# Optimization experiments

Measured on AMD Instinct MI355X. Metric: run time of the kernel, lower is better.

The kernel has to match this reference:

```python
import jax, jax.numpy as jnp
import numpy as np

N_ATOMS = 512
N_MOL = 16
HIDDEN = 128
FILTERS = 128
NUM_RBF = 50
CUTOFF = 10.0
N_LAYERS = 3


def setup_inputs() -> dict:
    key = jax.random.key(0)
    ks = jax.random.split(key, 20)
    s = 0.05
    inp = {
        "atomic_numbers": jax.random.randint(ks[0], (N_ATOMS,), 0, 100),
        "positions": jax.random.uniform(ks[1], (N_ATOMS, 3), jnp.float32) * CUTOFF,
        "batch": jnp.sort(jax.random.randint(ks[2], (N_ATOMS,), 0, N_MOL)),
        # parameters (linear weights stored as [in, out])
        "emb": jax.random.normal(ks[3], (100, HIDDEN), jnp.float32) * s,
        "fw1": jax.random.normal(ks[4], (N_LAYERS, NUM_RBF, FILTERS), jnp.float32) * s,
        "fb1": jnp.zeros((N_LAYERS, FILTERS), jnp.float32),
        "fw2": jax.random.normal(ks[5], (N_LAYERS, FILTERS, FILTERS), jnp.float32) * s,
        "fb2": jnp.zeros((N_LAYERS, FILTERS), jnp.float32),
        "d1w": jax.random.normal(ks[6], (N_LAYERS, HIDDEN, FILTERS), jnp.float32) * s,
        "d1b": jnp.zeros((N_LAYERS, FILTERS), jnp.float32),
        "d2w": jax.random.normal(ks[7], (N_LAYERS, FILTERS, HIDDEN), jnp.float32) * s,
        "d2b": jnp.zeros((N_LAYERS, HIDDEN), jnp.float32),
        "ow1": jax.random.normal(ks[8], (HIDDEN, HIDDEN // 2), jnp.float32) * s,
        "ob1": jnp.zeros((HIDDEN // 2,), jnp.float32),
        "ow2": jax.random.normal(ks[9], (HIDDEN // 2, 1), jnp.float32) * s,
        "ob2": jnp.zeros((1,), jnp.float32),
    }
    return inp


def _schnet_fwd(atomic_numbers, positions, batch, emb, fw1, fb1, fw2, fb2,
                d1w, d1b, d2w, d2b, ow1, ob1, ow2, ob2):
    N = positions.shape[0]
    x = emb[atomic_numbers]                                  # [N, H]

    # all-pairs distances (safe sqrt for the zero diagonal)
    diff = positions[:, None, :] - positions[None, :, :]     # [N, N, 3]
    d2 = jnp.sum(diff * diff, axis=-1)                       # [N, N]
    d = jnp.sqrt(jnp.where(d2 > 0, d2, 1.0))
    d = jnp.where(d2 > 0, d, 0.0)

    eye = jnp.eye(N, dtype=bool)
    valid = (~eye) & (d < CUTOFF)                            # no self-edges, within cutoff

    # gaussian RBF embedding of distances
    centers = jnp.linspace(0.0, CUTOFF, NUM_RBF)             # [R]
    width = CUTOFF / NUM_RBF
    rbf = jnp.exp(-((d[..., None] - centers) ** 2) / (2.0 * width * width))  # [N, N, R]

    # cosine cutoff envelope; zero on invalid edges -> messages identical to edge-list version
    env = 0.5 * (jnp.cos(d * jnp.pi / CUTOFF) + 1.0) * valid.astype(d.dtype)  # [N, N]

    for l in range(N_LAYERS):
        filt = jax.nn.silu(rbf @ fw1[l] + fb1[l]) @ fw2[l] + fb2[l]   # [N, N, F]
        filt = filt * env[..., None]
        xj = x @ d1w[l] + d1b[l]                                      # [N, F] source features
        # message[i,j] = xj[i] * filt[i,j]; scatter-add to destination j
        agg = jnp.einsum('if,ijf->jf', xj, filt)                      # [N, F]
        x = x + agg @ d2w[l] + d2b[l]

    # mean-pool atoms per molecule
    mol_sum = jax.ops.segment_sum(x, batch, num_segments=N_MOL)       # [M, H]
    counts = jax.ops.segment_sum(jnp.ones((N,), x.dtype), batch, num_segments=N_MOL)
    mol = mol_sum / jnp.clip(counts, 1.0)[:, None]

    h = jax.nn.silu(mol @ ow1 + ob1)
    return h @ ow2 + ob2                                              # [M, 1]


def reference(atomic_numbers, positions, batch, emb, fw1, fb1, fw2, fb2,
              d1w, d1b, d2w, d2b, ow1, ob1, ow2, ob2):
    return _schnet_fwd(atomic_numbers, positions, batch, emb, fw1, fb1, fw2, fb2,
                       d1w, d1b, d2w, d2b, ow1, ob1, ow2, ob2)
```

## Files before the change

### kernel.cpp

```cpp
#include <hip/hip_runtime.h>
#include <math.h>

#define N_ATOMS 512
#define N_MOL   16
#define HIDDEN  128
#define FILTERS 128
#define NUM_RBF 50
#define CUTOFF  10.0f
#define N_LAYERS 3

#define KB2    2048
#define NB2    (KB2 + 1)
#define TBPL   65
#define TBLK   (N_LAYERS * TBPL)
#define EMBB   16
#define PI_F   3.14159265358979f
#define DINV   204.8f
#define DSTEP  (CUTOFF / (float)KB2)
#define TAB_U4 ((NB2 * 64) / 4)

__device__ __forceinline__ unsigned short f2bf(float v) {
    unsigned u = __float_as_uint(v);
    u += 0x7fffu + ((u >> 16) & 1u);
    return (unsigned short)(u >> 16);
}

__global__ void __launch_bounds__(256) k_front(
        const int* __restrict__ an, const float* __restrict__ emb,
        const float* __restrict__ d1w, const float* __restrict__ d1b,
        const float* __restrict__ fw1, const float* __restrict__ fb1,
        const float* __restrict__ fw2, const float* __restrict__ fb2,
        float* __restrict__ x, unsigned short* __restrict__ xj,
        unsigned short* __restrict__ tab, float* __restrict__ molsum,
        int* __restrict__ done) {
    __shared__ float s_rbf[32][NUM_RBF];
    __shared__ __align__(16) float s_H[32][132];
    __shared__ __align__(16) float s_row[32][HIDDEN];
    __shared__ int   s_an[32];
    int bid = blockIdx.x, t = threadIdx.x;

    if (bid == 0) {
        for (int idx = t; idx < N_MOL * HIDDEN; idx += 256) molsum[idx] = 0.f;
        if (t < 4) done[t] = 0;
    }

    int cq = t & 31, ag = t >> 5;

    if (bid < TBLK) {
        int l = bid / TBPL, bx = bid - l * TBPL;
        int bin0 = bx * 32;
        const float* w1g = fw1 + (size_t)l * NUM_RBF * FILTERS;
        const float* w2g = fw2 + (size_t)l * FILTERS * FILTERS;
        for (int idx = t; idx < 32 * NUM_RBF; idx += 256) {
            int lb = idx / NUM_RBF, r = idx - lb * NUM_RBF;
            float dd = (bin0 + lb) * DSTEP;
            float cr = r * (CUTOFF / (float)(NUM_RBF - 1));
            float xx = dd - cr;
            s_rbf[lb][r] = __expf(-xx * xx * 12.5f);
        }
        __syncthreads();
        {
            float h[4][4];
            float4 bv = *(const float4*)(fb1 + (size_t)l * FILTERS + 4 * cq);
            float bva[4] = { bv.x, bv.y, bv.z, bv.w };
            #pragma unroll
            for (int aa = 0; aa < 4; aa++)
                #pragma unroll
                for (int cc = 0; cc < 4; cc++) h[aa][cc] = bva[cc];
            #pragma unroll 2
            for (int r = 0; r < NUM_RBF; r++) {
                float4 w = *(const float4*)(w1g + (size_t)r * FILTERS + 4 * cq);
                float wa[4] = { w.x, w.y, w.z, w.w };
                #pragma unroll
                for (int aa = 0; aa < 4; aa++) {
                    float rb = s_rbf[ag * 4 + aa][r];
                    #pragma unroll
                    for (int cc = 0; cc < 4; cc++) h[aa][cc] = fmaf(rb, wa[cc], h[aa][cc]);
                }
            }
            __syncthreads();
            #pragma unroll
            for (int aa = 0; aa < 4; aa++) {
                float4 sv;
                sv.x = h[aa][0] / (1.f + __expf(-h[aa][0]));
                sv.y = h[aa][1] / (1.f + __expf(-h[aa][1]));
                sv.z = h[aa][2] / (1.f + __expf(-h[aa][2]));
                sv.w = h[aa][3] / (1.f + __expf(-h[aa][3]));
                *(float4*)(&s_H[ag * 4 + aa][4 * cq]) = sv;
            }
        }
        __syncthreads();
        float o[4][4];
        float4 b2v = *(const float4*)(fb2 + (size_t)l * FILTERS + 4 * cq);
        float b2a[4] = { b2v.x, b2v.y, b2v.z, b2v.w };
        #pragma unroll
        for (int aa = 0; aa < 4; aa++)
            #pragma unroll
            for (int cc = 0; cc < 4; cc++) o[aa][cc] = b2a[cc];
        #pragma unroll 4
        for (int hh = 0; hh < FILTERS; hh += 2) {
            float4 wA = *(const float4*)(w2g + (size_t)hh * FILTERS + 4 * cq);
            float4 wB = *(const float4*)(w2g + (size_t)(hh + 1) * FILTERS + 4 * cq);
            float wa[4] = { wA.x, wA.y, wA.z, wA.w };
            float wb[4] = { wB.x, wB.y, wB.z, wB.w };
            #pragma unroll
            for (int aa = 0; aa < 4; aa++) {
                float2 hp = *(const float2*)(&s_H[ag * 4 + aa][hh]);
                #pragma unroll
                for (int cc = 0; cc < 4; cc++) {
                    o[aa][cc] = fmaf(hp.x, wa[cc], o[aa][cc]);
                    o[aa][cc] = fmaf(hp.y, wb[cc], o[aa][cc]);
                }
            }
        }
        size_t base = (size_t)l * NB2 * FILTERS;
        #pragma unroll
        for (int aa = 0; aa < 4; aa++) {
            int bin = bin0 + ag * 4 + aa;
            if (bin <= KB2) {
                float dd = bin * DSTEP;
                float env = (bin >= KB2) ? 0.f : 0.5f * (__cosf(dd * (PI_F / CUTOFF)) + 1.f);
                #pragma unroll
                for (int cp = 0; cp < 2; cp++) {
                    unsigned int pk = (unsigned)f2bf(o[aa][2 * cp] * env) |
                                      ((unsigned)f2bf(o[aa][2 * cp + 1] * env) << 16);
                    *(unsigned int*)(tab + base + (size_t)bin * FILTERS + 4 * cq + 2 * cp) = pk;
                }
            }
        }
    } else {
        int eb = bid - TBLK;
        int i0 = eb * 32;
        if (t < 32) s_an[t] = an[i0 + t];
        __syncthreads();
        for (int idx = t; idx < 32 * HIDDEN; idx += 256) {
            int a = idx >> 7, c = idx & 127;
            float v = emb[(size_t)s_an[a] * HIDDEN + c];
            s_row[a][c] = v;
            x[(size_t)(i0 + a) * HIDDEN + c] = v;
        }
        __syncthreads();
        float o[4][4];
        float4 bv = *(const float4*)(d1b + 4 * cq);
        float bva[4] = { bv.x, bv.y, bv.z, bv.w };
        #pragma unroll
        for (int aa = 0; aa < 4; aa++)
            #pragma unroll
            for (int cc = 0; cc < 4; cc++) o[aa][cc] = bva[cc];
        #pragma unroll 4
        for (int h = 0; h < HIDDEN; h += 2) {
            float4 wA = *(const float4*)(d1w + (size_t)h * FILTERS + 4 * cq);
            float4 wB = *(const float4*)(d1w + (size_t)(h + 1) * FILTERS + 4 * cq);
            float wa[4] = { wA.x, wA.y, wA.z, wA.w };
            float wb[4] = { wB.x, wB.y, wB.z, wB.w };
            #pragma unroll
            for (int aa = 0; aa < 4; aa++) {
                float2 hp = *(const float2*)(&s_row[ag * 4 + aa][h]);
                #pragma unroll
                for (int cc = 0; cc < 4; cc++) {
                    o[aa][cc] = fmaf(hp.x, wa[cc], o[aa][cc]);
                    o[aa][cc] = fmaf(hp.y, wb[cc], o[aa][cc]);
                }
            }
        }
        #pragma unroll
        for (int aa = 0; aa < 4; aa++) {
            int i = i0 + ag * 4 + aa;
            #pragma unroll
            for (int cp = 0; cp < 2; cp++) {
                unsigned int pk = (unsigned)f2bf(o[aa][2 * cp]) |
                                  ((unsigned)f2bf(o[aa][2 * cp + 1]) << 16);
                *(unsigned int*)(xj + (size_t)i * FILTERS + 4 * cq + 2 * cp) = pk;
            }
        }
    }
}

template<int LAST>
__global__ void __launch_bounds__(512) k_layer(const float* __restrict__ pos,
        const unsigned int* __restrict__ tabl, const unsigned int* __restrict__ xj_in,
        float* __restrict__ x, const float* __restrict__ w2, const float* __restrict__ b2,
        const float* __restrict__ w1n, const float* __restrict__ b1n,
        unsigned int* __restrict__ xj_out,
        const int* __restrict__ batch, float* __restrict__ molsum, int* __restrict__ done,
        const float* __restrict__ ow1, const float* __restrict__ ob1,
        const float* __restrict__ ow2, const float* __restrict__ ob2,
        float* __restrict__ out) {
    int j = blockIdx.x, t = threadIdx.x;
    int wv = t >> 6, e = t & 63;
    __shared__ unsigned short s_bin[N_ATOMS];
    __shared__ float s_part[8][FILTERS];
    __shared__ float s_red[4][FILTERS];
    __shared__ float s_agg[FILTERS];
    __shared__ float s_xn[HIDDEN];
    __shared__ int   s_tick;
    __shared__ float s_mol[16][HIDDEN];
    __shared__ float s_h[16][64];
    __shared__ int   s_c16[16];
    {
        float px = pos[3*t], py = pos[3*t+1], pz = pos[3*t+2];
        float ax = pos[3*j], ay = pos[3*j+1], az = pos[3*j+2];
        float d = sqrtf((px-ax)*(px-ax) + (py-ay)*(py-ay) + (pz-az)*(pz-az));
        unsigned int b = (t == j || d >= CUTOFF) ? KB2 : (unsigned)(int)fmaf(d, DINV, 0.5f);
        if (b > KB2) b = KB2;
        s_bin[t] = (unsigned short)b;
    }
    int c = t & 127, seg = t >> 7;
    float xold = (seg == 0) ? x[(size_t)j * HIDDEN + c] : 0.f;
    {
        const uint4* t4 = (const uint4*)tabl;
        int slice = (j >> 3) & 31;
        int q0 = slice * 1025;
        int qe = q0 + 1025; if (qe > TAB_U4) qe = TAB_U4;
        unsigned int acc = 0;
        for (int q = q0 + t; q < qe; q += 512) {
            uint4 w = t4[q];
            acc ^= w.x ^ w.y ^ w.z ^ w.w;
        }
        asm volatile("" :: "v"(acc));
    }
    __syncthreads();
    float ae = 0.f, ao = 0.f;
    int i0 = wv * 64;
    for (int ii = 0; ii < 64; ii += 8) {
        #pragma unroll
        for (int r = 0; r < 8; r++) {
            int bb = s_bin[i0 + ii + r];
            unsigned int xu = xj_in[(size_t)(i0 + ii + r) * 64 + e];
            unsigned int f  = tabl[(size_t)bb * 64 + e];
            float xe = __uint_as_float(xu << 16), xo = __uint_as_float(xu & 0xffff0000u);
            float pe = __uint_as_float(f << 16),  po = __uint_as_float(f & 0xffff0000u);
            ae = fmaf(xe, pe, ae);
            ao = fmaf(xo, po, ao);
        }
    }
    s_part[wv][2*e] = ae;  s_part[wv][2*e+1] = ao;
    __syncthreads();
    if (t < FILTERS) {
        float s = 0.f;
        #pragma unroll
        for (int w8 = 0; w8 < 8; w8++) s += s_part[w8][t];
        s_agg[t] = s;
    }
    __syncthreads();
    float v = 0.f;
    #pragma unroll 8
    for (int ff = seg * 32; ff < seg * 32 + 32; ff++)
        v = fmaf(s_agg[ff], w2[(size_t)ff * HIDDEN + c], v);
    s_red[seg][c] = v;
    __syncthreads();
    float xnew = 0.f;
    if (seg == 0) {
        xnew = xold + b2[c] + s_red[0][c] + s_red[1][c] + s_red[2][c] + s_red[3][c];
        x[(size_t)j * HIDDEN + c] = xnew;
        s_xn[c] = xnew;
    }
    __syncthreads();
    if (!LAST) {
        float a2 = 0.f;
        #pragma unroll 8
        for (int hh = seg * 32; hh < seg * 32 + 32; hh++)
            a2 = fmaf(s_xn[hh], w1n[(size_t)hh * FILTERS + c], a2);
        s_red[seg][c] = a2;
        __syncthreads();
        if (t < 64) {
            float v0 = b1n[2*t]   + s_red[0][2*t]   + s_red[1][2*t]   + s_red[2][2*t]   + s_red[3][2*t];
            float v1 = b1n[2*t+1] + s_red[0][2*t+1] + s_red[1][2*t+1] + s_red[2][2*t+1] + s_red[3][2*t+1];
            xj_out[(size_t)j * 64 + t] = (unsigned)f2bf(v0) | ((unsigned)f2bf(v1) << 16);
        }
    } else {
        if (seg == 0) atomicAdd(&molsum[(size_t)batch[j] * HIDDEN + c], xnew);
        __syncthreads();
        if (t == 0) s_tick = atomicAdd(&done[0], 1);
        __syncthreads();
        if (s_tick == (int)gridDim.x - 1) {
            if (t < 16) s_c16[t] = 0;
            __syncthreads();
            atomicAdd(&s_c16[batch[t]], 1);
            __syncthreads();
            #pragma unroll
            for (int mo = 0; mo < 4; mo++) {
                int m = mo * 4 + seg;
                float sv = atomicAdd(&molsum[(size_t)m * HIDDEN + c], 0.f);
                int cnt = s_c16[m];
                s_mol[m][c] = sv / (float)(cnt > 0 ? cnt : 1);
            }
            __syncthreads();
            #pragma unroll
            for (int rr = 0; rr < 2; rr++) {
                int o = t + rr * 512;
                int m = o >> 6, k = o & 63;
                float a = ob1[k];
                #pragma unroll 8
                for (int h = 0; h < HIDDEN; h++) a = fmaf(s_mol[m][h], ow1[h * 64 + k], a);
                s_h[m][k] = a / (1.f + __expf(-a));
            }
            __syncthreads();
            if (t < N_MOL) {
                float a = ob2[0];
                #pragma unroll 8
                for (int h = 0; h < 64; h++) a = fmaf(s_h[t][h], ow2[h], a);
                out[t] = a;
            }
        }
    }
}

extern "C" void kernel_launch(void* const* d_in, const int* in_sizes, int n_in,
                              void* d_out, int out_size, void* d_ws, size_t ws_size,
                              hipStream_t stream) {
    const int*   an    = (const int*)  d_in[0];
    const float* pos   = (const float*)d_in[1];
    const int*   batch = (const int*)  d_in[2];
    const float* emb   = (const float*)d_in[3];
    const float* fw1   = (const float*)d_in[4];
    const float* fb1   = (const float*)d_in[5];
    const float* fw2   = (const float*)d_in[6];
    const float* fb2   = (const float*)d_in[7];
    const float* d1w   = (const float*)d_in[8];
    const float* d1b   = (const float*)d_in[9];
    const float* d2w   = (const float*)d_in[10];
    const float* d2b   = (const float*)d_in[11];
    const float* ow1   = (const float*)d_in[12];
    const float* ob1   = (const float*)d_in[13];
    const float* ow2   = (const float*)d_in[14];
    const float* ob2   = (const float*)d_in[15];
    float* out = (float*)d_out;

    float*          x    = (float*)d_ws;
    unsigned int*   xj0  = (unsigned int*)(x + N_ATOMS * HIDDEN);
    unsigned int*   xj1  = xj0 + (size_t)N_ATOMS * 64;
    unsigned int*   xj2  = xj1 + (size_t)N_ATOMS * 64;
    unsigned short* tab  = (unsigned short*)(xj2 + (size_t)N_ATOMS * 64);
    float*          mols = (float*)(tab + (size_t)N_LAYERS * NB2 * FILTERS);
    int*            done = (int*)(mols + N_MOL * HIDDEN);

    k_front<<<TBLK + EMBB, 256, 0, stream>>>(
        an, emb, d1w, d1b, fw1, fb1, fw2, fb2, x, (unsigned short*)xj0, tab, mols, done);

    const unsigned int* t0 = (const unsigned int*)(tab + (size_t)0 * NB2 * FILTERS);
    const unsigned int* t1 = (const unsigned int*)(tab + (size_t)1 * NB2 * FILTERS);
    const unsigned int* t2 = (const unsigned int*)(tab + (size_t)2 * NB2 * FILTERS);

    k_layer<0><<<N_ATOMS, 512, 0, stream>>>(pos, t0, xj0, x,
        d2w + (size_t)0*FILTERS*HIDDEN, d2b + (size_t)0*HIDDEN,
        d1w + (size_t)1*HIDDEN*FILTERS, d1b + (size_t)1*FILTERS, xj1,
        batch, mols, done, ow1, ob1, ow2, ob2, out);
    k_layer<0><<<N_ATOMS, 512, 0, stream>>>(pos, t1, xj1, x,
        d2w + (size_t)1*FILTERS*HIDDEN, d2b + (size_t)1*HIDDEN,
        d1w + (size_t)2*HIDDEN*FILTERS, d1b + (size_t)2*FILTERS, xj2,
        batch, mols, done, ow1, ob1, ow2, ob2, out);
    k_layer<1><<<N_ATOMS, 512, 0, stream>>>(pos, t2, xj2, x,
        d2w + (size_t)2*FILTERS*HIDDEN, d2b + (size_t)2*HIDDEN,
        d1w, d1b, xj0,
        batch, mols, done, ow1, ob1, ow2, ob2, out);
}
```

Measured before the change: 59.54 us.

## Halve filter lookup table resolution and widen per-lane gather loads

Cuts the precomputed per-distance filter table from 2048 to 1024 bins, so fewer table blocks are launched and each layer's table footprint (and prefetch slice) is halved. The aggregation loop now has each lane load 8-byte uint2 chunks covering four filter channels, with two half-waves processing alternating source atoms and combining through a cross-lane shuffle. Coarser binning adds interpolation error to the distance-dependent filter, in exchange for less table construction work and more cache-friendly gathers.

```diff
diff --git a/kernel.cpp b/kernel.cpp
--- a/kernel.cpp
+++ b/kernel.cpp
@@ -9,21 +9,23 @@
 #define CUTOFF  10.0f
 #define N_LAYERS 3
 
-#define KB2    2048
-#define NB2    (KB2 + 1)
-#define TBPL   65
+#define KB1    1024
+#define NB1    (KB1 + 1)
+#define TBPL   33
 #define TBLK   (N_LAYERS * TBPL)
 #define EMBB   16
 #define PI_F   3.14159265358979f
-#define DINV   204.8f
-#define DSTEP  (CUTOFF / (float)KB2)
-#define TAB_U4 ((NB2 * 64) / 4)
+#define DINV   102.4f
+#define DSTEP  (CUTOFF / (float)KB1)
+#define TAB_U4 ((NB1 * FILTERS * 2) / 16)
 
 __device__ __forceinline__ unsigned short f2bf(float v) {
     unsigned u = __float_as_uint(v);
     u += 0x7fffu + ((u >> 16) & 1u);
     return (unsigned short)(u >> 16);
 }
+__device__ __forceinline__ float bflo(unsigned int u) { return __uint_as_float(u << 16); }
+__device__ __forceinline__ float bfhi(unsigned int u) { return __uint_as_float(u & 0xffff0000u); }
 
 __global__ void __launch_bounds__(256) k_front(
         const int* __restrict__ an, const float* __restrict__ emb,
@@ -113,13 +115,13 @@
                 }
             }
         }
-        size_t base = (size_t)l * NB2 * FILTERS;
+        size_t base = (size_t)l * NB1 * FILTERS;
         #pragma unroll
         for (int aa = 0; aa < 4; aa++) {
             int bin = bin0 + ag * 4 + aa;
-            if (bin <= KB2) {
+            if (bin <= KB1) {
                 float dd = bin * DSTEP;
-                float env = (bin >= KB2) ? 0.f : 0.5f * (__cosf(dd * (PI_F / CUTOFF)) + 1.f);
+                float env = (bin >= KB1) ? 0.f : 0.5f * (__cosf(dd * (PI_F / CUTOFF)) + 1.f);
                 #pragma unroll
                 for (int cp = 0; cp < 2; cp++) {
                     unsigned int pk = (unsigned)f2bf(o[aa][2 * cp] * env) |
@@ -201,17 +203,17 @@
         float px = pos[3*t], py = pos[3*t+1], pz = pos[3*t+2];
         float ax = pos[3*j], ay = pos[3*j+1], az = pos[3*j+2];
         float d = sqrtf((px-ax)*(px-ax) + (py-ay)*(py-ay) + (pz-az)*(pz-az));
-        unsigned int b = (t == j || d >= CUTOFF) ? KB2 : (unsigned)(int)fmaf(d, DINV, 0.5f);
-        if (b > KB2) b = KB2;
+        unsigned int b = (t == j || d >= CUTOFF) ? KB1 : (unsigned)(int)fmaf(d, DINV, 0.5f);
+        if (b > KB1) b = KB1;
         s_bin[t] = (unsigned short)b;
     }
     int c = t & 127, seg = t >> 7;
     float xold = (seg == 0) ? x[(size_t)j * HIDDEN + c] : 0.f;
     {
         const uint4* t4 = (const uint4*)tabl;
-        int slice = (j >> 3) & 31;
-        int q0 = slice * 1025;
-        int qe = q0 + 1025; if (qe > TAB_U4) qe = TAB_U4;
+        int slice = j & 31;
+        int q0 = slice * 513;
+        int qe = q0 + 513; if (qe > TAB_U4) qe = TAB_U4;
         unsigned int acc = 0;
         for (int q = q0 + t; q < qe; q += 512) {
             uint4 w = t4[q];
@@ -220,21 +222,36 @@
         asm volatile("" :: "v"(acc));
     }
     __syncthreads();
-    float ae = 0.f, ao = 0.f;
-    int i0 = wv * 64;
-    for (int ii = 0; ii < 64; ii += 8) {
-        #pragma unroll
-        for (int r = 0; r < 8; r++) {
-            int bb = s_bin[i0 + ii + r];
-            unsigned int xu = xj_in[(size_t)(i0 + ii + r) * 64 + e];
-            unsigned int f  = tabl[(size_t)bb * 64 + e];
-            float xe = __uint_as_float(xu << 16), xo = __uint_as_float(xu & 0xffff0000u);
-            float pe = __uint_as_float(f << 16),  po = __uint_as_float(f & 0xffff0000u);
-            ae = fmaf(xe, pe, ae);
-            ao = fmaf(xo, po, ao);
-        }
-    }
-    s_part[wv][2*e] = ae;  s_part[wv][2*e+1] = ao;
+    {
+        int h = e >> 5, cq4 = e & 31;
+        const uint2* tb2 = (const uint2*)tabl;
+        const uint2* xj2 = (const uint2*)xj_in;
+        float a0 = 0.f, a1 = 0.f, a2 = 0.f, a3 = 0.f;
+        int i0 = wv * 64;
+        for (int ii = 0; ii < 64; ii += 8) {
+            #pragma unroll
+            for (int r = 0; r < 8; r += 2) {
+                int i = i0 + ii + r + h;
+                int bb = s_bin[i];
+                uint2 f  = tb2[(size_t)bb * 32 + cq4];
+                uint2 xu = xj2[(size_t)i  * 32 + cq4];
+                a0 = fmaf(bflo(xu.x), bflo(f.x), a0);
+                a1 = fmaf(bfhi(xu.x), bfhi(f.x), a1);
+                a2 = fmaf(bflo(xu.y), bflo(f.y), a2);
+                a3 = fmaf(bfhi(xu.y), bfhi(f.y), a3);
+            }
+        }
+        a0 += __shfl_down(a0, 32, 64);
+        a1 += __shfl_down(a1, 32, 64);
+        a2 += __shfl_down(a2, 32, 64);
+        a3 += __shfl_down(a3, 32, 64);
+        if (h == 0) {
+            s_part[wv][4*cq4+0] = a0;
+            s_part[wv][4*cq4+1] = a1;
+            s_part[wv][4*cq4+2] = a2;
+            s_part[wv][4*cq4+3] = a3;
+        }
+    }
     __syncthreads();
     if (t < FILTERS) {
         float s = 0.f;
@@ -332,15 +349,15 @@
     unsigned int*   xj1  = xj0 + (size_t)N_ATOMS * 64;
     unsigned int*   xj2  = xj1 + (size_t)N_ATOMS * 64;
     unsigned short* tab  = (unsigned short*)(xj2 + (size_t)N_ATOMS * 64);
-    float*          mols = (float*)(tab + (size_t)N_LAYERS * NB2 * FILTERS);
+    float*          mols = (float*)(tab + (size_t)N_LAYERS * NB1 * FILTERS);
     int*            done = (int*)(mols + N_MOL * HIDDEN);
 
     k_front<<<TBLK + EMBB, 256, 0, stream>>>(
         an, emb, d1w, d1b, fw1, fb1, fw2, fb2, x, (unsigned short*)xj0, tab, mols, done);
 
-    const unsigned int* t0 = (const unsigned int*)(tab + (size_t)0 * NB2 * FILTERS);
-    const unsigned int* t1 = (const unsigned int*)(tab + (size_t)1 * NB2 * FILTERS);
-    const unsigned int* t2 = (const unsigned int*)(tab + (size_t)2 * NB2 * FILTERS);
+    const unsigned int* t0 = (const unsigned int*)(tab + (size_t)0 * NB1 * FILTERS);
+    const unsigned int* t1 = (const unsigned int*)(tab + (size_t)1 * NB1 * FILTERS);
+    const unsigned int* t2 = (const unsigned int*)(tab + (size_t)2 * NB1 * FILTERS);
 
     k_layer<0><<<N_ATOMS, 512, 0, stream>>>(pos, t0, xj0, x,
         d2w + (size_t)0*FILTERS*HIDDEN, d2b + (size_t)0*HIDDEN,
```

Result: slower. 65.07 us (+9.3%).
